# Kernel tuning notes

Hardware: AMD Instinct MI355X
Metric: run time of the kernel (lower is better)

The kernel has to match this reference:

```python
import jax, jax.numpy as jnp
import numpy as np
from jax import lax

N_GROUPS, TOP_K, CALIB_SCALE = 4, 3, 2.0


def setup_inputs() -> dict:
    key = jax.random.key(0)
    ks = jax.random.split(key, 32)
    d = {}
    d['x'] = jax.random.normal(ks[0], (64, 64, 8192), jnp.float32)
    d['conv_weight'] = jax.random.normal(ks[1], (64, 64, 3), jnp.float32) * 0.05
    d['bias'] = jax.random.normal(ks[2], (64,), jnp.float32) * 0.05
    d['grads'] = jax.random.normal(ks[3], (12288,), jnp.float32) * 0.01
    d['q_ema'] = jax.random.normal(ks[4], (4416,), jnp.float32) * 0.1
    d['ctrl_w'] = jax.random.normal(ks[5], (64, 192), jnp.float32) * 0.07
    d['ctrl_b'] = jnp.zeros((64,), jnp.float32)
    d['gp_w'] = jax.random.normal(ks[6], (64, 65), jnp.float32) * 0.1
    d['gp_b'] = jnp.zeros((64,), jnp.float32)
    d['gt_w'] = jax.random.normal(ks[7], (64, 64), jnp.float32) * 0.1
    d['gt_b'] = jnp.zeros((64,), jnp.float32)
    d['ln_g'] = jnp.ones((64,), jnp.float32)
    d['ln_b'] = jnp.zeros((64,), jnp.float32)
    d['ccin_w'] = jax.random.normal(ks[8], (64, 64), jnp.float32) * 0.05
    d['ccin_b'] = jnp.zeros((64,), jnp.float32)
    d['ck_w'] = jax.random.normal(ks[9], (3, 64), jnp.float32) * 0.05
    d['ck_b'] = jnp.zeros((3,), jnp.float32)
    d['cb_w'] = jax.random.normal(ks[10], (1, 64), jnp.float32) * 0.05
    d['cb_b'] = jnp.zeros((1,), jnp.float32)
    d['cf_w'] = jax.random.normal(ks[11], (1, 64), jnp.float32) * 0.05
    d['cf_b'] = jnp.zeros((1,), jnp.float32)
    d['tau_w'] = jax.random.normal(ks[12], (1, 64), jnp.float32) * 0.1
    d['tau_b'] = jnp.zeros((1,), jnp.float32)
    W = jax.random.normal(ks[13], (4, 1104, 32), jnp.float32)
    d['mem_W'] = W / jnp.linalg.norm(W, axis=1, keepdims=True)  # column-normalized codebook
    d['temp_logit'] = jnp.zeros((4,), jnp.float32)
    return d


def reference(x, conv_weight, bias, grads, q_ema, ctrl_w, ctrl_b, gp_w, gp_b,
              gt_w, gt_b, ln_g, ln_b, ccin_w, ccin_b, ck_w, ck_b, cb_w, cb_b,
              cf_w, cf_b, tau_w, tau_b, mem_W, temp_logit):
    C_out, C_in, K = conv_weight.shape
    cpg = C_out // N_GROUPS
    cin_tot, k_tot = C_out * C_in, C_out * K
    shift = 0.0  # shift_magnitude

    # --- controller: grads -> calibration query q ---
    g = grads.reshape(C_out, C_in * K)
    h = jax.nn.silu(g @ ctrl_w.T + ctrl_b)
    gn = jnp.linalg.norm(g, axis=-1, keepdims=True)
    z = jax.nn.sigmoid(jnp.concatenate([h, gn], -1) @ gp_w.T + gp_b)
    h_t = jax.nn.silu(h @ gt_w.T + gt_b)
    hm = (1.0 - z) * h + z * h_t
    mu = hm.mean(-1, keepdims=True)
    var = ((hm - mu) ** 2).mean(-1, keepdims=True)
    h = ln_g * (hm - mu) / jnp.sqrt(var + 1e-5) + ln_b

    w_cin = jnp.tanh(h @ ccin_w.T + ccin_b) * CALIB_SCALE   # [C_out, C_in]
    w_k = jnp.tanh(h @ ck_w.T + ck_b) * CALIB_SCALE         # [C_out, K]
    b_r = jnp.tanh(h @ cb_w.T + cb_b)[:, 0] * CALIB_SCALE   # [C_out]
    f_r = jnp.tanh(h @ cf_w.T + cf_b)[:, 0] * CALIB_SCALE   # [C_out]
    tau = jax.nn.sigmoid(h @ tau_w.T + tau_b).mean() * 0.5 + 0.5

    q = jnp.concatenate([w_cin.reshape(-1), w_k.reshape(-1), b_r, f_r])
    q = 0.7 * q + 0.3 * lax.stop_gradient(q_ema)

    # --- channel-grouped codebook retrieval (trigger path) ---
    qd = lax.stop_gradient(q)
    q_groups = jnp.concatenate([
        qd[:cin_tot].reshape(N_GROUPS, cpg * C_in),
        qd[cin_tot:cin_tot + k_tot].reshape(N_GROUPS, cpg * K),
        qd[cin_tot + k_tot:cin_tot + k_tot + C_out].reshape(N_GROUPS, cpg),
        qd[cin_tot + k_tot + C_out:].reshape(N_GROUPS, cpg)], axis=1)  # [G, gq]
    temp = (jax.nn.sigmoid(temp_logit) * 0.6 + 0.2) / (1.0 + shift)     # [G]
    att = jnp.einsum('gd,gdm->gm', q_groups, mem_W)
    att = jax.nn.softmax(att / (temp[:, None] + 1e-8), axis=1)
    v, idx = lax.top_k(att, TOP_K)                                      # [G, k]
    gath = jnp.take_along_axis(mem_W, idx[:, None, :], axis=2)          # [G, gq, k]
    retrieved = (gath * v[:, None, :]).sum(-1)                          # [G, gq]

    s0, s1, s2 = cpg * C_in, cpg * (C_in + K), cpg * (C_in + K + 1)
    retrieved_global = jnp.concatenate([
        retrieved[:, :s0].reshape(-1),
        retrieved[:, s0:s1].reshape(-1),
        retrieved[:, s1:s2].reshape(-1),
        retrieved[:, s2:].reshape(-1)])
    q = tau * q + (1.0 - tau) * lax.stop_gradient(retrieved_global)

    # --- split q and modulate conv ---
    w_cin = q[:cin_tot].reshape(C_out, C_in)
    w_k = q[cin_tot:cin_tot + k_tot].reshape(C_out, K)
    b_c = q[cin_tot + k_tot:cin_tot + k_tot + C_out]
    f_c = q[cin_tot + k_tot + C_out:]

    w = conv_weight * (1.0 + w_cin)[:, :, None] * (1.0 + w_k)[:, None, :]
    pad = ((K - 1) * 1 + 1) // 2  # receptive_field // 2 (dilation=1)
    out = lax.conv_general_dilated(x, w, window_strides=(1,),
                                   padding=[(pad, pad)], rhs_dilation=(1,),
                                   dimension_numbers=('NCH', 'OIH', 'NCH'))
    out = out + (bias * (1.0 + b_c))[None, :, None]
    out = out * (1.0 + f_c)[None, :, None]
    return out
```

## Files before the change

kernel.cpp:

```cpp
#include <hip/hip_runtime.h>
#include <math.h>

typedef __attribute__((ext_vector_type(8))) short bf16x8;
typedef __attribute__((ext_vector_type(4))) float f32x4;

__device__ __forceinline__ float sigmoidf_(float x) { return 1.f / (1.f + expf(-x)); }

__device__ __forceinline__ unsigned short f2bf(float f) {
  unsigned int u = __float_as_uint(f);
  u += 0x7fffu + ((u >> 16) & 1u);
  return (unsigned short)(u >> 16);
}

#define WS_QG    0
#define WS_TAU   4416
#define WS_V     4420
#define WS_IDX   4432
#define WS_BEFF  4448
#define WS_SEFF  4512
#define WS_WFRAG 4608

__global__ __launch_bounds__(1024) void kA(
    const float* __restrict__ grads, const float* __restrict__ ctrl_w, const float* __restrict__ ctrl_b,
    const float* __restrict__ gp_w, const float* __restrict__ gp_b,
    const float* __restrict__ gt_w, const float* __restrict__ gt_b,
    const float* __restrict__ ln_g, const float* __restrict__ ln_b,
    const float* __restrict__ ccin_w, const float* __restrict__ ccin_b,
    const float* __restrict__ ck_w, const float* __restrict__ ck_b,
    const float* __restrict__ cb_w, const float* __restrict__ cb_b,
    const float* __restrict__ cf_w, const float* __restrict__ cf_b,
    const float* __restrict__ tau_w, const float* __restrict__ tau_b,
    const float* __restrict__ q_ema, float* __restrict__ ws) {
  __shared__ float rawA[8514];
  __shared__ float sh_h[64 * 65];
  __shared__ float gnp[64 * 17];
  __shared__ float taup[64];
  const int tid = threadIdx.x;
  const int j = tid & 63;
  const int wv = tid >> 6;
  const int i0 = wv * 4;
  const int i0u = __builtin_amdgcn_readfirstlane(i0);

  float acc[4] = {0.f, 0.f, 0.f, 0.f};
  for (int hh = 0; hh < 2; ++hh) {
    const int d0 = hh * 96;
    for (int t = tid; t < 6144; t += 1024) {
      int jj = t / 96, dl = t - jj * 96;
      rawA[dl * 66 + jj] = ctrl_w[jj * 192 + d0 + dl];
    }
    __syncthreads();
    const float* g0 = grads + i0u * 192 + d0;
#pragma unroll 8
    for (int dl = 0; dl < 96; ++dl) {
      float wvv = rawA[dl * 66 + j];
      acc[0] += wvv * g0[dl];
      acc[1] += wvv * g0[192 + dl];
      acc[2] += wvv * g0[384 + dl];
      acc[3] += wvv * g0[576 + dl];
    }
    __syncthreads();
  }
  {
    float cb_ = ctrl_b[j];
#pragma unroll
    for (int ii = 0; ii < 4; ++ii) {
      float s = acc[ii] + cb_;
      sh_h[(i0 + ii) * 65 + j] = s * sigmoidf_(s);
    }
  }
  {
    int gi = tid >> 4, seg = tid & 15;
    const float* gr = grads + gi * 192 + seg * 12;
    float ss = 0.f;
#pragma unroll
    for (int m = 0; m < 12; ++m) { float v = gr[m]; ss += v * v; }
    gnp[gi * 17 + seg] = ss;
  }
  __syncthreads();
  if (tid < 64) {
    float s = 0.f;
#pragma unroll
    for (int seg = 0; seg < 16; ++seg) s += gnp[tid * 17 + seg];
    gnp[tid * 17 + 16] = sqrtf(s);
  }
  for (int t = tid; t < 4096; t += 1024) rawA[(t & 63) * 66 + (t >> 6)] = gt_w[t];
  for (int t = tid; t < 4160; t += 1024) {
    int jj = t / 65, dd = t - jj * 65;
    rawA[4224 + dd * 66 + jj] = gp_w[t];
  }
  __syncthreads();

  float hm[4];
  {
    float zacc[4] = {0.f, 0.f, 0.f, 0.f}, tacc[4] = {0.f, 0.f, 0.f, 0.f};
#pragma unroll 4
    for (int d = 0; d < 64; ++d) {
      float gtv = rawA[d * 66 + j];
      float gpv = rawA[4224 + d * 66 + j];
#pragma unroll
      for (int ii = 0; ii < 4; ++ii) {
        float hv = sh_h[(i0 + ii) * 65 + d];
        tacc[ii] += hv * gtv;
        zacc[ii] += hv * gpv;
      }
    }
    float gplast = rawA[4224 + 64 * 66 + j];
    float zb = gp_b[j], tb = gt_b[j];
#pragma unroll
    for (int ii = 0; ii < 4; ++ii) {
      float gn_ = gnp[(i0 + ii) * 17 + 16];
      float zs = zacc[ii] + gn_ * gplast + zb;
      float ts = tacc[ii] + tb;
      float z = sigmoidf_(zs);
      float ht = ts * sigmoidf_(ts);
      hm[ii] = (1.f - z) * sh_h[(i0 + ii) * 65 + j] + z * ht;
    }
  }
  __syncthreads();
#pragma unroll
  for (int ii = 0; ii < 4; ++ii) sh_h[(i0 + ii) * 65 + j] = hm[ii];
  __syncthreads();

  {
    float lg = ln_g[j], lb = ln_b[j];
#pragma unroll
    for (int ii = 0; ii < 4; ++ii) {
      float x = sh_h[(i0 + ii) * 65 + j];
      float s = x;
#pragma unroll
      for (int off = 32; off; off >>= 1) s += __shfl_xor(s, off);
      float mu = s * (1.f / 64.f);
      float dv = x - mu;
      float v2 = dv * dv;
#pragma unroll
      for (int off = 32; off; off >>= 1) v2 += __shfl_xor(v2, off);
      float invs = 1.f / sqrtf(v2 * (1.f / 64.f) + 1e-5f);
      sh_h[(i0 + ii) * 65 + j] = lg * dv * invs + lb;
    }
  }
  for (int t = tid; t < 4096; t += 1024) rawA[(t & 63) * 66 + (t >> 6)] = ccin_w[t];
  if (tid < 384) {
    int c = tid >> 6, d = tid & 63;
    float v = (c < 3) ? ck_w[c * 64 + d] : (c == 3) ? cb_w[d] : (c == 4) ? cf_w[d] : tau_w[d];
    rawA[4224 + c * 64 + d] = v;
  }
  __syncthreads();

  {
    float cb_ = ccin_b[j];
    float s4[4] = {0.f, 0.f, 0.f, 0.f};
#pragma unroll 4
    for (int d = 0; d < 64; ++d) {
      float cv = rawA[d * 66 + j];
#pragma unroll
      for (int ii = 0; ii < 4; ++ii) s4[ii] += sh_h[(i0 + ii) * 65 + d] * cv;
    }
#pragma unroll
    for (int ii = 0; ii < 4; ++ii) {
      int i = i0 + ii;
      float val = 2.f * tanhf(s4[ii] + cb_);
      ws[WS_QG + (i >> 4) * 1104 + (i & 15) * 64 + j] = 0.7f * val + 0.3f * q_ema[i * 64 + j];
    }
  }
  if (wv < 6) {
    int i = j;
    float s = 0.f;
    const float* er = rawA + 4224 + wv * 64;
#pragma unroll 4
    for (int d = 0; d < 64; ++d) s += sh_h[i * 65 + d] * er[d];
    if (wv < 3) {
      float val = 2.f * tanhf(s + ck_b[wv]);
      ws[WS_QG + (i >> 4) * 1104 + 1024 + (i & 15) * 3 + wv] = 0.7f * val + 0.3f * q_ema[4096 + i * 3 + wv];
    } else if (wv == 3) {
      float val = 2.f * tanhf(s + cb_b[0]);
      ws[WS_QG + (i >> 4) * 1104 + 1072 + (i & 15)] = 0.7f * val + 0.3f * q_ema[4288 + i];
    } else if (wv == 4) {
      float val = 2.f * tanhf(s + cf_b[0]);
      ws[WS_QG + (i >> 4) * 1104 + 1088 + (i & 15)] = 0.7f * val + 0.3f * q_ema[4352 + i];
    } else {
      taup[i] = sigmoidf_(s + tau_b[0]);
    }
  }
  __syncthreads();
  if (tid < 64) {
    float t_ = taup[tid];
#pragma unroll
    for (int off = 32; off; off >>= 1) t_ += __shfl_xor(t_, off);
    if (tid == 0) ws[WS_TAU] = (t_ * (1.f / 64.f)) * 0.5f + 0.5f;
  }
}

__global__ __launch_bounds__(512) void kB(
    const float* __restrict__ mem_W, const float* __restrict__ temp_logit, float* __restrict__ ws) {
  __shared__ float qs[1104];
  __shared__ float part[8 * 32];
  const int tid = threadIdx.x;
  const int g = blockIdx.x;
  const int wave = tid >> 6, lane = tid & 63;
  const int dl = lane >> 3, m4 = lane & 7;
  for (int t = tid; t < 1104; t += 512) qs[t] = ws[WS_QG + g * 1104 + t];
  __syncthreads();
  const float* mwg = mem_W + (size_t)g * 1104 * 32;
  float4 a = {0.f, 0.f, 0.f, 0.f};
  for (int it = 0; it < 18; ++it) {
    int d = it * 64 + wave * 8 + dl;
    if (d < 1104) {
      float4 v4 = *(const float4*)(mwg + (size_t)d * 32 + m4 * 4);
      float qv = qs[d];
      a.x += qv * v4.x; a.y += qv * v4.y; a.z += qv * v4.z; a.w += qv * v4.w;
    }
  }
#pragma unroll
  for (int off = 8; off <= 32; off <<= 1) {
    a.x += __shfl_xor(a.x, off); a.y += __shfl_xor(a.y, off);
    a.z += __shfl_xor(a.z, off); a.w += __shfl_xor(a.w, off);
  }
  if (dl == 0) {
    float* p = part + wave * 32 + m4 * 4;
    p[0] = a.x; p[1] = a.y; p[2] = a.z; p[3] = a.w;
  }
  __syncthreads();
  if (tid < 32) {
    int m = tid;
    float att = 0.f;
#pragma unroll
    for (int w = 0; w < 8; ++w) att += part[w * 32 + m];
    float temp = 0.6f * sigmoidf_(temp_logit[g]) + 0.2f;
    att /= (temp + 1e-8f);
    float mx = att;
#pragma unroll
    for (int off = 16; off; off >>= 1) mx = fmaxf(mx, __shfl_xor(mx, off, 32));
    float e = expf(att - mx);
    float s = e;
#pragma unroll
    for (int off = 16; off; off >>= 1) s += __shfl_xor(s, off, 32);
    float p = e / s;
    for (int t = 0; t < 3; ++t) {
      float bp = p; int bm = m;
#pragma unroll
      for (int off = 16; off; off >>= 1) {
        float op = __shfl_xor(bp, off, 32);
        int om = __shfl_xor(bm, off, 32);
        if (op > bp || (op == bp && om < bm)) { bp = op; bm = om; }
      }
      if (m == 0) { ws[WS_V + g * 3 + t] = bp; ((int*)ws)[WS_IDX + g * 3 + t] = bm; }
      if (m == bm) p = -1.f;
    }
  }
}

__global__ __launch_bounds__(256) void kD(
    const float* __restrict__ mem_W, const float* __restrict__ conv_weight,
    const float* __restrict__ bias, float* __restrict__ ws) {
  __shared__ float qc1[4][64];
  __shared__ float qk1[4][4];
  const int tid = threadIdx.x;
  const int wv = tid >> 6, l = tid & 63;
  const int co = blockIdx.x * 4 + wv;
  const int g = co >> 4;
  const float tau = ws[WS_TAU];
  const float v0 = ws[WS_V + g * 3 + 0], v1 = ws[WS_V + g * 3 + 1], v2 = ws[WS_V + g * 3 + 2];
  const int x0 = ((const int*)ws)[WS_IDX + g * 3 + 0];
  const int x1 = ((const int*)ws)[WS_IDX + g * 3 + 1];
  const int x2 = ((const int*)ws)[WS_IDX + g * 3 + 2];
  const float* mwg = mem_W + (size_t)g * 1104 * 32;
  const float* qg = ws + WS_QG + g * 1104;
  {
    int d = (co & 15) * 64 + l;
    float r = v0 * mwg[(size_t)d * 32 + x0] + v1 * mwg[(size_t)d * 32 + x1] + v2 * mwg[(size_t)d * 32 + x2];
    qc1[wv][l] = 1.f + tau * qg[d] + (1.f - tau) * r;
  }
  if (l < 3) {
    int d = 1024 + (co & 15) * 3 + l;
    float r = v0 * mwg[(size_t)d * 32 + x0] + v1 * mwg[(size_t)d * 32 + x1] + v2 * mwg[(size_t)d * 32 + x2];
    qk1[wv][l] = 1.f + tau * qg[d] + (1.f - tau) * r;
  }
  if (l == 3) {
    int d = 1072 + (co & 15);
    float r = v0 * mwg[(size_t)d * 32 + x0] + v1 * mwg[(size_t)d * 32 + x1] + v2 * mwg[(size_t)d * 32 + x2];
    float qb = tau * qg[d] + (1.f - tau) * r;
    ws[WS_BEFF + co] = bias[co] * (1.f + qb);
  }
  if (l == 4) {
    int d = 1088 + (co & 15);
    float r = v0 * mwg[(size_t)d * 32 + x0] + v1 * mwg[(size_t)d * 32 + x1] + v2 * mwg[(size_t)d * 32 + x2];
    ws[WS_SEFF + co] = 1.f + tau * qg[d] + (1.f - tau) * r;
  }
  __syncthreads();
  unsigned short* wfrag = (unsigned short*)(ws + WS_WFRAG);
  const float* cwc = conv_weight + co * 192;
#pragma unroll
  for (int kk = 0; kk < 3; ++kk) {
    int e = kk * 64 + l;
    int s = e >> 5, hi = (e >> 3) & 3, jj = e & 7;
    int f = s * 2048 + (co >> 4) * 512 + (16 * hi + (co & 15)) * 8 + jj;
    wfrag[f] = f2bf(cwc[l * 3 + kk] * qc1[wv][l] * qk1[wv][kk]);
  }
}

__global__ __launch_bounds__(256, 3) void k3_mfma(
    const float* __restrict__ x, const unsigned short* __restrict__ wfrag,
    const float* __restrict__ beff, const float* __restrict__ seff,
    float* __restrict__ out) {
  __shared__ unsigned short xs[258 * 72];
  const int tid = threadIdx.x;
  const int w = tid >> 6, l = tid & 63;
  const int n = blockIdx.y;
  const int l0 = blockIdx.x * 256;

  bf16x8 wf[6];
#pragma unroll
  for (int s = 0; s < 6; ++s)
    wf[s] = *(const bf16x8*)(wfrag + s * 2048 + w * 512 + l * 8);

  {
    const int ci = 16 * w + (l & 15);
    const float* row = x + ((size_t)(n * 64 + ci)) * 8192 + l0;
    unsigned short* col = xs + ci;
#pragma unroll
    for (int cc = 0; cc < 16; ++cc) {
      int c = 4 * cc + (l >> 4);
      float4 v = *(const float4*)(row + 4 * c);
      col[(1 + 4 * c) * 72] = f2bf(v.x);
      col[(2 + 4 * c) * 72] = f2bf(v.y);
      col[(3 + 4 * c) * 72] = f2bf(v.z);
      col[(4 + 4 * c) * 72] = f2bf(v.w);
    }
    if (tid < 128) {
      int ci2 = tid >> 1, side = tid & 1;
      int gp = side ? (l0 + 256) : (l0 - 1);
      float v = (gp >= 0 && gp < 8192) ? x[((size_t)(n * 64 + ci2)) * 8192 + gp] : 0.f;
      xs[(side ? 257 : 0) * 72 + ci2] = f2bf(v);
    }
  }
  __syncthreads();

  f32x4 acc[16];
#pragma unroll
  for (int t = 0; t < 16; ++t) acc[t] = (f32x4){0.f, 0.f, 0.f, 0.f};

#pragma unroll
  for (int s = 0; s < 6; ++s) {
    const int kk = s >> 1;
    const int coff = (s & 1) * 32 + 8 * (l >> 4);
    const int pbase = (l & 15) + kk;
#pragma unroll
    for (int nt = 0; nt < 16; ++nt) {
      bf16x8 a = *(const bf16x8*)(xs + (nt * 16 + pbase) * 72 + coff);
      acc[nt] = __builtin_amdgcn_mfma_f32_16x16x32_bf16(a, wf[s], acc[nt], 0, 0, 0);
    }
  }

  const int co = 16 * w + (l & 15);
  const float be = beff[co], se = seff[co];
  float* orow = out + ((size_t)(n * 64 + co)) * 8192 + l0 + (l >> 4) * 4;
#pragma unroll
  for (int nt = 0; nt < 16; ++nt) {
    float4 o;
    o.x = se * (acc[nt][0] + be);
    o.y = se * (acc[nt][1] + be);
    o.z = se * (acc[nt][2] + be);
    o.w = se * (acc[nt][3] + be);
    *(float4*)(orow + nt * 16) = o;
  }
}

extern "C" void kernel_launch(void* const* d_in, const int* in_sizes, int n_in,
                              void* d_out, int out_size, void* d_ws, size_t ws_size,
                              hipStream_t stream) {
  const float* x = (const float*)d_in[0];
  const float* conv_weight = (const float*)d_in[1];
  const float* bias = (const float*)d_in[2];
  const float* grads = (const float*)d_in[3];
  const float* q_ema = (const float*)d_in[4];
  const float* ctrl_w = (const float*)d_in[5];
  const float* ctrl_b = (const float*)d_in[6];
  const float* gp_w = (const float*)d_in[7];
  const float* gp_b = (const float*)d_in[8];
  const float* gt_w = (const float*)d_in[9];
  const float* gt_b = (const float*)d_in[10];
  const float* ln_g = (const float*)d_in[11];
  const float* ln_b = (const float*)d_in[12];
  const float* ccin_w = (const float*)d_in[13];
  const float* ccin_b = (const float*)d_in[14];
  const float* ck_w = (const float*)d_in[15];
  const float* ck_b = (const float*)d_in[16];
  const float* cb_w = (const float*)d_in[17];
  const float* cb_b = (const float*)d_in[18];
  const float* cf_w = (const float*)d_in[19];
  const float* cf_b = (const float*)d_in[20];
  const float* tau_w = (const float*)d_in[21];
  const float* tau_b = (const float*)d_in[22];
  const float* mem_W = (const float*)d_in[23];
  const float* temp_logit = (const float*)d_in[24];

  float* ws = (float*)d_ws;

  hipLaunchKernelGGL(kA, dim3(1), dim3(1024), 0, stream,
                     grads, ctrl_w, ctrl_b, gp_w, gp_b, gt_w, gt_b, ln_g, ln_b,
                     ccin_w, ccin_b, ck_w, ck_b, cb_w, cb_b, cf_w, cf_b,
                     tau_w, tau_b, q_ema, ws);
  hipLaunchKernelGGL(kB, dim3(4), dim3(512), 0, stream, mem_W, temp_logit, ws);
  hipLaunchKernelGGL(kD, dim3(16), dim3(256), 0, stream, mem_W, conv_weight, bias, ws);
  hipLaunchKernelGGL(k3_mfma, dim3(32, 64), dim3(256), 0, stream,
                     x, (const unsigned short*)(ws + WS_WFRAG), ws + WS_BEFF, ws + WS_SEFF,
                     (float*)d_out);
}
```

Measured before the change: 110.6 us.

## Fuse retrieval with weight prep and restructure conv as shifted MFMA outputs

```diff
diff --git a/kernel.cpp b/kernel.cpp
--- a/kernel.cpp
+++ b/kernel.cpp
@@ -11,11 +11,12 @@
   u += 0x7fffu + ((u >> 16) & 1u);
   return (unsigned short)(u >> 16);
 }
+__device__ __forceinline__ float bf2f(unsigned short u) {
+  return __uint_as_float(((unsigned int)u) << 16);
+}
 
 #define WS_QG    0
 #define WS_TAU   4416
-#define WS_V     4420
-#define WS_IDX   4432
 #define WS_BEFF  4448
 #define WS_SEFF  4512
 #define WS_WFRAG 4608
@@ -190,10 +191,16 @@
   }
 }
 
-__global__ __launch_bounds__(512) void kB(
-    const float* __restrict__ mem_W, const float* __restrict__ temp_logit, float* __restrict__ ws) {
+__global__ __launch_bounds__(512) void kBD(
+    const float* __restrict__ mem_W, const float* __restrict__ temp_logit,
+    const float* __restrict__ conv_weight, const float* __restrict__ bias,
+    float* __restrict__ ws) {
   __shared__ float qs[1104];
   __shared__ float part[8 * 32];
+  __shared__ float sv[3];
+  __shared__ int sidx[3];
+  __shared__ float qc1[16][64];
+  __shared__ float qk1[16][3];
   const int tid = threadIdx.x;
   const int g = blockIdx.x;
   const int wave = tid >> 6, lane = tid & 63;
@@ -201,23 +208,25 @@
   for (int t = tid; t < 1104; t += 512) qs[t] = ws[WS_QG + g * 1104 + t];
   __syncthreads();
   const float* mwg = mem_W + (size_t)g * 1104 * 32;
-  float4 a = {0.f, 0.f, 0.f, 0.f};
-  for (int it = 0; it < 18; ++it) {
-    int d = it * 64 + wave * 8 + dl;
-    if (d < 1104) {
-      float4 v4 = *(const float4*)(mwg + (size_t)d * 32 + m4 * 4);
-      float qv = qs[d];
-      a.x += qv * v4.x; a.y += qv * v4.y; a.z += qv * v4.z; a.w += qv * v4.w;
-    }
-  }
-#pragma unroll
-  for (int off = 8; off <= 32; off <<= 1) {
-    a.x += __shfl_xor(a.x, off); a.y += __shfl_xor(a.y, off);
-    a.z += __shfl_xor(a.z, off); a.w += __shfl_xor(a.w, off);
-  }
-  if (dl == 0) {
-    float* p = part + wave * 32 + m4 * 4;
-    p[0] = a.x; p[1] = a.y; p[2] = a.z; p[3] = a.w;
+  {
+    float4 a = {0.f, 0.f, 0.f, 0.f};
+    for (int it = 0; it < 18; ++it) {
+      int d = it * 64 + wave * 8 + dl;
+      if (d < 1104) {
+        float4 v4 = *(const float4*)(mwg + (size_t)d * 32 + m4 * 4);
+        float qv = qs[d];
+        a.x += qv * v4.x; a.y += qv * v4.y; a.z += qv * v4.z; a.w += qv * v4.w;
+      }
+    }
+#pragma unroll
+    for (int off = 8; off <= 32; off <<= 1) {
+      a.x += __shfl_xor(a.x, off); a.y += __shfl_xor(a.y, off);
+      a.z += __shfl_xor(a.z, off); a.w += __shfl_xor(a.w, off);
+    }
+    if (dl == 0) {
+      float* p = part + wave * 32 + m4 * 4;
+      p[0] = a.x; p[1] = a.y; p[2] = a.z; p[3] = a.w;
+    }
   }
   __syncthreads();
   if (tid < 32) {
@@ -243,125 +252,163 @@
         int om = __shfl_xor(bm, off, 32);
         if (op > bp || (op == bp && om < bm)) { bp = op; bm = om; }
       }
-      if (m == 0) { ws[WS_V + g * 3 + t] = bp; ((int*)ws)[WS_IDX + g * 3 + t] = bm; }
+      if (m == 0) { sv[t] = bp; sidx[t] = bm; }
       if (m == bm) p = -1.f;
     }
   }
-}
-
-__global__ __launch_bounds__(256) void kD(
-    const float* __restrict__ mem_W, const float* __restrict__ conv_weight,
-    const float* __restrict__ bias, float* __restrict__ ws) {
-  __shared__ float qc1[4][64];
-  __shared__ float qk1[4][4];
-  const int tid = threadIdx.x;
-  const int wv = tid >> 6, l = tid & 63;
-  const int co = blockIdx.x * 4 + wv;
-  const int g = co >> 4;
+  __syncthreads();
   const float tau = ws[WS_TAU];
-  const float v0 = ws[WS_V + g * 3 + 0], v1 = ws[WS_V + g * 3 + 1], v2 = ws[WS_V + g * 3 + 2];
-  const int x0 = ((const int*)ws)[WS_IDX + g * 3 + 0];
-  const int x1 = ((const int*)ws)[WS_IDX + g * 3 + 1];
-  const int x2 = ((const int*)ws)[WS_IDX + g * 3 + 2];
-  const float* mwg = mem_W + (size_t)g * 1104 * 32;
-  const float* qg = ws + WS_QG + g * 1104;
-  {
-    int d = (co & 15) * 64 + l;
-    float r = v0 * mwg[(size_t)d * 32 + x0] + v1 * mwg[(size_t)d * 32 + x1] + v2 * mwg[(size_t)d * 32 + x2];
-    qc1[wv][l] = 1.f + tau * qg[d] + (1.f - tau) * r;
-  }
-  if (l < 3) {
-    int d = 1024 + (co & 15) * 3 + l;
-    float r = v0 * mwg[(size_t)d * 32 + x0] + v1 * mwg[(size_t)d * 32 + x1] + v2 * mwg[(size_t)d * 32 + x2];
-    qk1[wv][l] = 1.f + tau * qg[d] + (1.f - tau) * r;
-  }
-  if (l == 3) {
-    int d = 1072 + (co & 15);
-    float r = v0 * mwg[(size_t)d * 32 + x0] + v1 * mwg[(size_t)d * 32 + x1] + v2 * mwg[(size_t)d * 32 + x2];
-    float qb = tau * qg[d] + (1.f - tau) * r;
-    ws[WS_BEFF + co] = bias[co] * (1.f + qb);
-  }
-  if (l == 4) {
-    int d = 1088 + (co & 15);
-    float r = v0 * mwg[(size_t)d * 32 + x0] + v1 * mwg[(size_t)d * 32 + x1] + v2 * mwg[(size_t)d * 32 + x2];
-    ws[WS_SEFF + co] = 1.f + tau * qg[d] + (1.f - tau) * r;
+  const float v0 = sv[0], v1 = sv[1], v2 = sv[2];
+  const int x0 = sidx[0], x1 = sidx[1], x2 = sidx[2];
+#pragma unroll
+  for (int rr = 0; rr < 2; ++rr) {
+    int cl = wave + 8 * rr;
+    int co = 16 * g + cl;
+    {
+      int d = cl * 64 + lane;
+      float r = v0 * mwg[(size_t)d * 32 + x0] + v1 * mwg[(size_t)d * 32 + x1] + v2 * mwg[(size_t)d * 32 + x2];
+      qc1[cl][lane] = 1.f + tau * qs[d] + (1.f - tau) * r;
+    }
+    if (lane < 3) {
+      int d = 1024 + cl * 3 + lane;
+      float r = v0 * mwg[(size_t)d * 32 + x0] + v1 * mwg[(size_t)d * 32 + x1] + v2 * mwg[(size_t)d * 32 + x2];
+      qk1[cl][lane] = 1.f + tau * qs[d] + (1.f - tau) * r;
+    }
+    if (lane == 3) {
+      int d = 1072 + cl;
+      float r = v0 * mwg[(size_t)d * 32 + x0] + v1 * mwg[(size_t)d * 32 + x1] + v2 * mwg[(size_t)d * 32 + x2];
+      float qb = tau * qs[d] + (1.f - tau) * r;
+      ws[WS_BEFF + co] = bias[co] * (1.f + qb);
+    }
+    if (lane == 4) {
+      int d = 1088 + cl;
+      float r = v0 * mwg[(size_t)d * 32 + x0] + v1 * mwg[(size_t)d * 32 + x1] + v2 * mwg[(size_t)d * 32 + x2];
+      ws[WS_SEFF + co] = 1.f + tau * qs[d] + (1.f - tau) * r;
+    }
   }
   __syncthreads();
   unsigned short* wfrag = (unsigned short*)(ws + WS_WFRAG);
-  const float* cwc = conv_weight + co * 192;
-#pragma unroll
-  for (int kk = 0; kk < 3; ++kk) {
-    int e = kk * 64 + l;
+  for (int idx = tid; idx < 3072; idx += 512) {
+    int cl = idx / 192, rem = idx - cl * 192;
+    int kk = rem >> 6, ci = rem & 63;
+    int co = 16 * g + cl;
+    float val = conv_weight[(co * 64 + ci) * 3 + kk] * qc1[cl][ci] * qk1[cl][kk];
+    int e = kk * 64 + ci;
     int s = e >> 5, hi = (e >> 3) & 3, jj = e & 7;
-    int f = s * 2048 + (co >> 4) * 512 + (16 * hi + (co & 15)) * 8 + jj;
-    wfrag[f] = f2bf(cwc[l * 3 + kk] * qc1[wv][l] * qk1[wv][kk]);
-  }
-}
-
-__global__ __launch_bounds__(256, 3) void k3_mfma(
+    wfrag[s * 2048 + g * 512 + (16 * hi + cl) * 8 + jj] = f2bf(val);
+  }
+}
+
+__global__ __launch_bounds__(256, 4) void k3_y(
     const float* __restrict__ x, const unsigned short* __restrict__ wfrag,
     const float* __restrict__ beff, const float* __restrict__ seff,
     float* __restrict__ out) {
-  __shared__ unsigned short xs[258 * 72];
+  __shared__ unsigned short xs[128 * 66];
+  __shared__ float lhal[64], rhal[64];
   const int tid = threadIdx.x;
   const int w = tid >> 6, l = tid & 63;
+  const int g = l >> 4, c16 = l & 15;
   const int n = blockIdx.y;
-  const int l0 = blockIdx.x * 256;
+  const int l0 = blockIdx.x * 128;
 
   bf16x8 wf[6];
 #pragma unroll
   for (int s = 0; s < 6; ++s)
     wf[s] = *(const bf16x8*)(wfrag + s * 2048 + w * 512 + l * 8);
 
-  {
-    const int ci = 16 * w + (l & 15);
-    const float* row = x + ((size_t)(n * 64 + ci)) * 8192 + l0;
-    unsigned short* col = xs + ci;
-#pragma unroll
-    for (int cc = 0; cc < 16; ++cc) {
-      int c = 4 * cc + (l >> 4);
-      float4 v = *(const float4*)(row + 4 * c);
-      col[(1 + 4 * c) * 72] = f2bf(v.x);
-      col[(2 + 4 * c) * 72] = f2bf(v.y);
-      col[(3 + 4 * c) * 72] = f2bf(v.z);
-      col[(4 + 4 * c) * 72] = f2bf(v.w);
-    }
-    if (tid < 128) {
-      int ci2 = tid >> 1, side = tid & 1;
-      int gp = side ? (l0 + 256) : (l0 - 1);
-      float v = (gp >= 0 && gp < 8192) ? x[((size_t)(n * 64 + ci2)) * 8192 + gp] : 0.f;
-      xs[(side ? 257 : 0) * 72 + ci2] = f2bf(v);
-    }
-  }
-  __syncthreads();
-
-  f32x4 acc[16];
-#pragma unroll
-  for (int t = 0; t < 16; ++t) acc[t] = (f32x4){0.f, 0.f, 0.f, 0.f};
-
-#pragma unroll
-  for (int s = 0; s < 6; ++s) {
-    const int kk = s >> 1;
-    const int coff = (s & 1) * 32 + 8 * (l >> 4);
-    const int pbase = (l & 15) + kk;
-#pragma unroll
-    for (int nt = 0; nt < 16; ++nt) {
-      bf16x8 a = *(const bf16x8*)(xs + (nt * 16 + pbase) * 72 + coff);
-      acc[nt] = __builtin_amdgcn_mfma_f32_16x16x32_bf16(a, wf[s], acc[nt], 0, 0, 0);
-    }
-  }
-
-  const int co = 16 * w + (l & 15);
+  if (tid < 128) {
+    int side = tid >> 6, ci = tid & 63;
+    int gp = side ? (l0 + 128) : (l0 - 1);
+    float v = (gp >= 0 && gp < 8192) ? x[((size_t)(n * 64 + ci)) * 8192 + gp] : 0.f;
+    (side ? rhal : lhal)[ci] = v;
+  }
+
+  {
+    const float* xb = x + (size_t)n * 64 * 8192 + l0;
+#pragma unroll
+    for (int s2 = 0; s2 < 2; ++s2) {
+      int cp = 8 * w + 4 * s2 + g;
+      const float* r0 = xb + (size_t)(2 * cp) * 8192;
+      const float* r1 = r0 + 8192;
+#pragma unroll
+      for (int rep = 0; rep < 2; ++rep) {
+        int p = 4 * c16 + 64 * rep;
+        float4 va = *(const float4*)(r0 + p);
+        float4 vb = *(const float4*)(r1 + p);
+        unsigned u0 = (unsigned)f2bf(va.x) | ((unsigned)f2bf(vb.x) << 16);
+        unsigned u1 = (unsigned)f2bf(va.y) | ((unsigned)f2bf(vb.y) << 16);
+        unsigned u2 = (unsigned)f2bf(va.z) | ((unsigned)f2bf(vb.z) << 16);
+        unsigned u3 = (unsigned)f2bf(va.w) | ((unsigned)f2bf(vb.w) << 16);
+        *(unsigned*)&xs[(p + 0) * 66 + 2 * cp] = u0;
+        *(unsigned*)&xs[(p + 1) * 66 + 2 * cp] = u1;
+        *(unsigned*)&xs[(p + 2) * 66 + 2 * cp] = u2;
+        *(unsigned*)&xs[(p + 3) * 66 + 2 * cp] = u3;
+      }
+    }
+  }
+  __syncthreads();
+
+  float s0 = 0.f, s2s = 0.f;
+#pragma unroll
+  for (int s = 0; s < 2; ++s) {
+#pragma unroll
+    for (int jj = 0; jj < 8; ++jj) {
+      int ci = 32 * s + 8 * g + jj;
+      s0  += bf2f((unsigned short)wf[s][jj]) * lhal[ci];
+      s2s += bf2f((unsigned short)wf[4 + s][jj]) * rhal[ci];
+    }
+  }
+  s0 += __shfl_xor(s0, 16);  s0 += __shfl_xor(s0, 32);
+  s2s += __shfl_xor(s2s, 16); s2s += __shfl_xor(s2s, 32);
+  float carry0 = s0;
+
+  f32x4 o[8];
+#pragma unroll
+  for (int nt = 0; nt < 8; ++nt) o[nt] = (f32x4){0.f, 0.f, 0.f, 0.f};
+
+#pragma unroll
+  for (int nt = 0; nt < 8; ++nt) {
+    union { bf16x8 v; unsigned u[4]; } A0, A1;
+    const int rbase = (16 * nt + c16) * 66;
+#pragma unroll
+    for (int k = 0; k < 4; ++k) {
+      A0.u[k] = *(const unsigned*)&xs[rbase + 8 * g + 2 * k];
+      A1.u[k] = *(const unsigned*)&xs[rbase + 32 + 8 * g + 2 * k];
+    }
+    o[nt] = __builtin_amdgcn_mfma_f32_16x16x32_bf16(A0.v, wf[2], o[nt], 0, 0, 0);
+    o[nt] = __builtin_amdgcn_mfma_f32_16x16x32_bf16(A1.v, wf[3], o[nt], 0, 0, 0);
+    f32x4 y0 = (f32x4){0.f, 0.f, 0.f, 0.f};
+    f32x4 y2 = (f32x4){0.f, 0.f, 0.f, 0.f};
+    y0 = __builtin_amdgcn_mfma_f32_16x16x32_bf16(A0.v, wf[0], y0, 0, 0, 0);
+    y0 = __builtin_amdgcn_mfma_f32_16x16x32_bf16(A1.v, wf[1], y0, 0, 0, 0);
+    y2 = __builtin_amdgcn_mfma_f32_16x16x32_bf16(A0.v, wf[4], y2, 0, 0, 0);
+    y2 = __builtin_amdgcn_mfma_f32_16x16x32_bf16(A1.v, wf[5], y2, 0, 0, 0);
+    float sh = __shfl(y0[3], (l - 16) & 63);
+    o[nt][0] += (g == 0) ? carry0 : sh;
+    o[nt][1] += y0[0];
+    o[nt][2] += y0[1];
+    o[nt][3] += y0[2];
+    carry0 = sh;
+    float b0 = __shfl(y2[0], (l + 16) & 63);
+    o[nt][0] += y2[1];
+    o[nt][1] += y2[2];
+    o[nt][2] += y2[3];
+    o[nt][3] += (g < 3) ? b0 : 0.f;
+    if (nt > 0) o[nt - 1][3] += (g == 3) ? b0 : 0.f;
+  }
+  o[7][3] += (g == 3) ? s2s : 0.f;
+
+  const int co = 16 * w + c16;
   const float be = beff[co], se = seff[co];
-  float* orow = out + ((size_t)(n * 64 + co)) * 8192 + l0 + (l >> 4) * 4;
-#pragma unroll
-  for (int nt = 0; nt < 16; ++nt) {
-    float4 o;
-    o.x = se * (acc[nt][0] + be);
-    o.y = se * (acc[nt][1] + be);
-    o.z = se * (acc[nt][2] + be);
-    o.w = se * (acc[nt][3] + be);
-    *(float4*)(orow + nt * 16) = o;
+  float* orow = out + ((size_t)(n * 64 + co)) * 8192 + l0 + 4 * g;
+#pragma unroll
+  for (int nt = 0; nt < 8; ++nt) {
+    float4 ov;
+    ov.x = se * (o[nt][0] + be);
+    ov.y = se * (o[nt][1] + be);
+    ov.z = se * (o[nt][2] + be);
+    ov.w = se * (o[nt][3] + be);
+    *(float4*)(orow + nt * 16) = ov;
   }
 }
 
@@ -400,9 +447,8 @@
                      grads, ctrl_w, ctrl_b, gp_w, gp_b, gt_w, gt_b, ln_g, ln_b,
                      ccin_w, ccin_b, ck_w, ck_b, cb_w, cb_b, cf_w, cf_b,
                      tau_w, tau_b, q_ema, ws);
-  hipLaunchKernelGGL(kB, dim3(4), dim3(512), 0, stream, mem_W, temp_logit, ws);
-  hipLaunchKernelGGL(kD, dim3(16), dim3(256), 0, stream, mem_W, conv_weight, bias, ws);
-  hipLaunchKernelGGL(k3_mfma, dim3(32, 64), dim3(256), 0, stream,
+  hipLaunchKernelGGL(kBD, dim3(4), dim3(512), 0, stream, mem_W, temp_logit, conv_weight, bias, ws);
+  hipLaunchKernelGGL(k3_y, dim3(64, 64), dim3(256), 0, stream,
                      x, (const unsigned short*)(ws + WS_WFRAG), ws + WS_BEFF, ws + WS_SEFF,
                      (float*)d_out);
 }
```

After: 123.1 us. 1.11x slower.
